# Kernel tuning notes

Hardware: AMD Instinct MI355X
Metric: run time of the kernel (lower is better)

Reference implementation:

```python
import jax, jax.numpy as jnp
import numpy as np

K = 9          # kernel_size
PAD = 4        # padding
N_OUT, C_IN = 32, 32


def setup_inputs() -> dict:
    key = jax.random.key(0)
    k1, k2, k3, k4, k5 = jax.random.split(key, 5)
    x = jax.random.normal(k1, (16, C_IN, 192, 192), jnp.float32)
    sx = jax.random.uniform(k2, (N_OUT, C_IN), jnp.float32, 0.2, 4.0)
    sy = jax.random.uniform(k3, (N_OUT, C_IN), jnp.float32, 0.2, 4.0)
    th = jax.random.uniform(k4, (N_OUT, C_IN), jnp.float32, 0.0, 2.0 * np.pi)
    weight = jnp.stack([sx, sy, th], axis=-1)          # [N, C, 3]
    bias = jax.random.normal(k5, (N_OUT,), jnp.float32) * 0.01
    return {"x": x, "weight": weight, "bias": bias}


def _gaussian_kernels(weight, k):
    # weight: [N, C, 3] -> normalized anisotropic Gaussian kernels [N, C, k, k]
    sx, sy = weight[..., 0], weight[..., 1]
    rad = weight[..., 2] / 180.0 * jnp.pi          # matches theta/180*pi in source
    c, s = jnp.cos(rad), jnp.sin(rad)
    sx2, sy2 = sx * sx, sy * sy
    # Sigma = U diag(sx^2, sy^2) U^T, U = [[c,-s],[s,c]] -> Sigma = [[a,b],[b,d]]
    a = c * c * sx2 + s * s * sy2
    b = c * s * (sx2 - sy2)
    d = s * s * sx2 + c * c * sy2
    det = a * d - b * b
    ia, ib, id_ = d / det, -b / det, a / det       # closed-form 2x2 inverse
    ax = jnp.arange(k, dtype=jnp.float32) - k // 2
    xx = ax[None, :]                               # x varies along columns
    yy = ax[:, None]                               # y varies along rows
    # quadratic form: ia*x^2 + 2*ib*x*y + id*y^2, broadcast to [N, C, k, k]
    q = (ia[..., None, None] * (xx * xx)
         + 2.0 * ib[..., None, None] * (xx * yy)
         + id_[..., None, None] * (yy * yy))
    ker = jnp.exp(-0.5 * q)
    return ker / jnp.sum(ker, axis=(-2, -1), keepdims=True)


def reference(x, weight, bias):
    w = _gaussian_kernels(weight, K)               # [N, C, K, K]
    out = jax.lax.conv_general_dilated(
        x, w, window_strides=(1, 1), padding=[(PAD, PAD), (PAD, PAD)],
        dimension_numbers=("NCHW", "OIHW", "NCHW"))
    return out + bias[None, :, None, None]
```

## Files before the change

### kernel.cpp

```cpp
#include <hip/hip_runtime.h>

#define H 192
#define W 192
#define CIN 32
#define NOUT 32
#define NB 16
#define PADI 4

#define HT 16
#define WTL 16
#define RROWS 24
#define RCOLS 24

typedef __attribute__((ext_vector_type(8))) short bf16x8;
typedef __attribute__((ext_vector_type(4))) float f32x4;

__device__ __forceinline__ unsigned short f2bf(float f) {
    union { float f; unsigned int u; } v; v.f = f;
    unsigned int r = v.u + 0x7fffu + ((v.u >> 16) & 1u);
    return (unsigned short)(r >> 16);
}

__global__ void genw_kernel(const float* __restrict__ wp, unsigned short* __restrict__ W2g) {
    int idx = blockIdx.x * blockDim.x + threadIdx.x;
    if (idx >= NOUT * CIN) return;
    int o = idx / CIN;
    float sx = wp[idx * 3 + 0], sy = wp[idx * 3 + 1], th = wp[idx * 3 + 2];
    float rad = th / 180.0f * 3.14159265358979323846f;
    float co = cosf(rad), si = sinf(rad);
    float sx2 = sx * sx, sy2 = sy * sy;
    float a = co * co * sx2 + si * si * sy2;
    float b = co * si * (sx2 - sy2);
    float d = si * si * sx2 + co * co * sy2;
    float det = a * d - b * b;
    float ia = d / det, ib = -b / det, idd = a / det;
    float ker[81];
    float sum = 0.0f;
    for (int ky = 0; ky < 9; ky++) {
        float yy = (float)(ky - 4);
        for (int kx = 0; kx < 9; kx++) {
            float xx = (float)(kx - 4);
            float q = ia * xx * xx + 2.0f * ib * xx * yy + idd * yy * yy;
            float v = expf(-0.5f * q);
            ker[ky * 9 + kx] = v;
            sum += v;
        }
    }
    float inv = 1.0f / sum;
    int i = idx % CIN;
    int mt = o >> 4, m = o & 15, quad = i >> 3, j = i & 7;
    for (int tap = 0; tap < 81; tap++) {
        W2g[((((mt * 81 + tap) * 4 + quad) * 16 + m) << 3) + j] = f2bf(ker[tap] * inv);
    }
}

__global__ __launch_bounds__(256, 4) void conv_kernel(
    const float* __restrict__ x, const unsigned short* __restrict__ W2g,
    const float* __restrict__ bias, float* __restrict__ out)
{
    __shared__ __align__(16) unsigned short ldsx[4 * RROWS * RCOLS * 8];

    const int t = threadIdx.x;
    const int bid = blockIdx.x;
    const int wb = bid % (W / WTL);
    const int hb = (bid / (W / WTL)) % (H / HT);
    const int n  = bid / ((W / WTL) * (H / HT));
    const int row0 = hb * HT - PADI;
    const int col0 = wb * WTL - PADI;
    const float* xn = x + (size_t)n * CIN * H * W;

    #pragma unroll
    for (int it = 0; it < (4 * RROWS * RCOLS) / 256; ++it) {
        int idx = it * 256 + t;
        int w = idx % RCOLS;
        int r = (idx / RCOLS) % RROWS;
        int quad = idx / (RCOLS * RROWS);
        int row = row0 + r, col = col0 + w;
        unsigned int d[4] = {0u, 0u, 0u, 0u};
        if ((unsigned)row < (unsigned)H && (unsigned)col < (unsigned)W) {
            const float* p = xn + ((size_t)(quad * 8) * H + row) * W + col;
            #pragma unroll
            for (int k = 0; k < 4; k++) {
                float v0 = p[(size_t)(2 * k) * H * W];
                float v1 = p[(size_t)(2 * k + 1) * H * W];
                d[k] = (unsigned int)f2bf(v0) | ((unsigned int)f2bf(v1) << 16);
            }
        }
        *(uint4*)&ldsx[(size_t)idx * 8] = make_uint4(d[0], d[1], d[2], d[3]);
    }
    __syncthreads();

    const int wave = t >> 6;
    const int lane = t & 63;
    const int l15 = lane & 15;
    const int quad4 = lane >> 4;
    const int mt = wave & 1;
    const int rbase = (wave >> 1) * 8;

    f32x4 acc[8];
    #pragma unroll
    for (int i = 0; i < 8; i++) acc[i] = (f32x4){0.f, 0.f, 0.f, 0.f};

    const bf16x8* __restrict__ Wp = (const bf16x8*)W2g;

    for (int dx = 0; dx < 9; dx++) {
        bf16x8 Afr[9];
        #pragma unroll
        for (int dy = 0; dy < 9; dy++) {
            int tap = dy * 9 + dx;
            Afr[dy] = Wp[((mt * 81 + tap) * 4 + quad4) * 16 + l15];
        }
        #pragma unroll
        for (int rr = 0; rr < 16; rr++) {
            const int ldsrow = rbase + rr;
            const bf16x8 bfrag =
                *(const bf16x8*)&ldsx[(size_t)(((quad4 * RROWS + ldsrow) * RCOLS) + (l15 + dx)) * 8];
            #pragma unroll
            for (int dy = 0; dy < 9; dy++) {
                const int orr = rr - dy;
                if (orr >= 0 && orr < 8) {
                    acc[orr] = __builtin_amdgcn_mfma_f32_16x16x32_bf16(
                        Afr[dy], bfrag, acc[orr], 0, 0, 0);
                }
            }
        }
    }

    float* outn = out + (size_t)n * NOUT * H * W;
    float bb[4];
    #pragma unroll
    for (int reg = 0; reg < 4; reg++) bb[reg] = bias[mt * 16 + quad4 * 4 + reg];
    #pragma unroll
    for (int orr = 0; orr < 8; orr++) {
        const int row = hb * HT + rbase + orr;
        const int col = wb * WTL + l15;
        #pragma unroll
        for (int reg = 0; reg < 4; reg++) {
            const int och = mt * 16 + quad4 * 4 + reg;
            outn[((size_t)och * H + row) * W + col] = acc[orr][reg] + bb[reg];
        }
    }
}

extern "C" void kernel_launch(void* const* d_in, const int* in_sizes, int n_in,
                              void* d_out, int out_size, void* d_ws, size_t ws_size,
                              hipStream_t stream) {
    const float* x    = (const float*)d_in[0];
    const float* wp   = (const float*)d_in[1];
    const float* bias = (const float*)d_in[2];
    float* out = (float*)d_out;
    unsigned short* W2g = (unsigned short*)d_ws;

    genw_kernel<<<4, 256, 0, stream>>>(wp, W2g);
    const int blocks = NB * (H / HT) * (W / WTL);
    conv_kernel<<<blocks, 256, 0, stream>>>(x, W2g, bias, out);
}
```

Measured before the change: 211.3 us.

## Parallelize weight generation, swizzle blocks, batch global loads, double-buffer weight fragments

```diff
diff --git a/kernel.cpp b/kernel.cpp
--- a/kernel.cpp
+++ b/kernel.cpp
@@ -22,35 +22,40 @@
 }
 
 __global__ void genw_kernel(const float* __restrict__ wp, unsigned short* __restrict__ W2g) {
-    int idx = blockIdx.x * blockDim.x + threadIdx.x;
-    if (idx >= NOUT * CIN) return;
-    int o = idx / CIN;
-    float sx = wp[idx * 3 + 0], sy = wp[idx * 3 + 1], th = wp[idx * 3 + 2];
+    const int b = blockIdx.x;
+    const int o = b >> 5;
+    const int i = b & 31;
+    const int t = threadIdx.x;
+
+    float sx = wp[b * 3 + 0], sy = wp[b * 3 + 1], th = wp[b * 3 + 2];
     float rad = th / 180.0f * 3.14159265358979323846f;
     float co = cosf(rad), si = sinf(rad);
     float sx2 = sx * sx, sy2 = sy * sy;
     float a = co * co * sx2 + si * si * sy2;
-    float b = co * si * (sx2 - sy2);
+    float bb = co * si * (sx2 - sy2);
     float d = si * si * sx2 + co * co * sy2;
-    float det = a * d - b * b;
-    float ia = d / det, ib = -b / det, idd = a / det;
-    float ker[81];
-    float sum = 0.0f;
-    for (int ky = 0; ky < 9; ky++) {
-        float yy = (float)(ky - 4);
-        for (int kx = 0; kx < 9; kx++) {
-            float xx = (float)(kx - 4);
-            float q = ia * xx * xx + 2.0f * ib * xx * yy + idd * yy * yy;
-            float v = expf(-0.5f * q);
-            ker[ky * 9 + kx] = v;
-            sum += v;
-        }
+    float det = a * d - bb * bb;
+    float ia = d / det, ib = -bb / det, idd = a / det;
+
+    const int tap = t;
+    float e = 0.0f;
+    if (tap < 81) {
+        float xx = (float)(tap % 9 - 4);
+        float yy = (float)(tap / 9 - 4);
+        float q = ia * xx * xx + 2.0f * ib * xx * yy + idd * yy * yy;
+        e = expf(-0.5f * q);
     }
-    float inv = 1.0f / sum;
-    int i = idx % CIN;
-    int mt = o >> 4, m = o & 15, quad = i >> 3, j = i & 7;
-    for (int tap = 0; tap < 81; tap++) {
-        W2g[((((mt * 81 + tap) * 4 + quad) * 16 + m) << 3) + j] = f2bf(ker[tap] * inv);
+    float s = e;
+    #pragma unroll
+    for (int off = 32; off > 0; off >>= 1) s += __shfl_down(s, off);
+    __shared__ float ws[2];
+    if ((t & 63) == 0) ws[t >> 6] = s;
+    __syncthreads();
+    float total = ws[0] + ws[1];
+
+    if (tap < 81) {
+        int mt = o >> 4, m = o & 15, quad = i >> 3, j = i & 7;
+        W2g[((((mt * 81 + tap) * 4 + quad) * 16 + m) << 3) + j] = f2bf(e / total);
     }
 }
 
@@ -61,7 +66,7 @@
     __shared__ __align__(16) unsigned short ldsx[4 * RROWS * RCOLS * 8];
 
     const int t = threadIdx.x;
-    const int bid = blockIdx.x;
+    const int bid = (blockIdx.x & 7) * 288 + (blockIdx.x >> 3);
     const int wb = bid % (W / WTL);
     const int hb = (bid / (W / WTL)) % (H / HT);
     const int n  = bid / ((W / WTL) * (H / HT));
@@ -69,26 +74,31 @@
     const int col0 = wb * WTL - PADI;
     const float* xn = x + (size_t)n * CIN * H * W;
 
+    float v[9][8];
     #pragma unroll
-    for (int it = 0; it < (4 * RROWS * RCOLS) / 256; ++it) {
+    for (int it = 0; it < 9; ++it) {
         int idx = it * 256 + t;
         int w = idx % RCOLS;
         int r = (idx / RCOLS) % RROWS;
         int quad = idx / (RCOLS * RROWS);
         int row = row0 + r, col = col0 + w;
-        unsigned int d[4] = {0u, 0u, 0u, 0u};
+        #pragma unroll
+        for (int k = 0; k < 8; k++) v[it][k] = 0.0f;
         if ((unsigned)row < (unsigned)H && (unsigned)col < (unsigned)W) {
             const float* p = xn + ((size_t)(quad * 8) * H + row) * W + col;
             #pragma unroll
-            for (int k = 0; k < 4; k++) {
-                float v0 = p[(size_t)(2 * k) * H * W];
-                float v1 = p[(size_t)(2 * k + 1) * H * W];
-                d[k] = (unsigned int)f2bf(v0) | ((unsigned int)f2bf(v1) << 16);
-            }
+            for (int k = 0; k < 8; k++) v[it][k] = p[(size_t)k * H * W];
         }
+    }
+    #pragma unroll
+    for (int it = 0; it < 9; ++it) {
+        int idx = it * 256 + t;
+        unsigned int d[4];
+        #pragma unroll
+        for (int k = 0; k < 4; k++)
+            d[k] = (unsigned int)f2bf(v[it][2 * k]) | ((unsigned int)f2bf(v[it][2 * k + 1]) << 16);
         *(uint4*)&ldsx[(size_t)idx * 8] = make_uint4(d[0], d[1], d[2], d[3]);
     }
-    __syncthreads();
 
     const int wave = t >> 6;
     const int lane = t & 63;
@@ -97,30 +107,38 @@
     const int mt = wave & 1;
     const int rbase = (wave >> 1) * 8;
 
+    const bf16x8* __restrict__ Wp = (const bf16x8*)W2g;
+
+    bf16x8 A[2][9];
+    #pragma unroll
+    for (int dy = 0; dy < 9; dy++)
+        A[0][dy] = Wp[((mt * 81 + dy * 9 + 0) * 4 + quad4) * 16 + l15];
+
+    __syncthreads();
+
     f32x4 acc[8];
     #pragma unroll
     for (int i = 0; i < 8; i++) acc[i] = (f32x4){0.f, 0.f, 0.f, 0.f};
 
-    const bf16x8* __restrict__ Wp = (const bf16x8*)W2g;
+    const unsigned short* bptr = &ldsx[(size_t)(((quad4 * RROWS + rbase) * RCOLS) + l15) * 8];
 
+    #pragma unroll
     for (int dx = 0; dx < 9; dx++) {
-        bf16x8 Afr[9];
-        #pragma unroll
-        for (int dy = 0; dy < 9; dy++) {
-            int tap = dy * 9 + dx;
-            Afr[dy] = Wp[((mt * 81 + tap) * 4 + quad4) * 16 + l15];
+        const int cur = dx & 1, nxt = cur ^ 1;
+        if (dx < 8) {
+            #pragma unroll
+            for (int dy = 0; dy < 9; dy++)
+                A[nxt][dy] = Wp[((mt * 81 + dy * 9 + (dx + 1)) * 4 + quad4) * 16 + l15];
         }
         #pragma unroll
         for (int rr = 0; rr < 16; rr++) {
-            const int ldsrow = rbase + rr;
-            const bf16x8 bfrag =
-                *(const bf16x8*)&ldsx[(size_t)(((quad4 * RROWS + ldsrow) * RCOLS) + (l15 + dx)) * 8];
+            const bf16x8 bfrag = *(const bf16x8*)&bptr[(size_t)(rr * RCOLS + dx) * 8];
             #pragma unroll
             for (int dy = 0; dy < 9; dy++) {
                 const int orr = rr - dy;
                 if (orr >= 0 && orr < 8) {
                     acc[orr] = __builtin_amdgcn_mfma_f32_16x16x32_bf16(
-                        Afr[dy], bfrag, acc[orr], 0, 0, 0);
+                        A[cur][dy], bfrag, acc[orr], 0, 0, 0);
                 }
             }
         }
@@ -151,7 +169,7 @@
     float* out = (float*)d_out;
     unsigned short* W2g = (unsigned short*)d_ws;
 
-    genw_kernel<<<4, 256, 0, stream>>>(wp, W2g);
+    genw_kernel<<<NOUT * CIN, 128, 0, stream>>>(wp, W2g);
     const int blocks = NB * (H / HT) * (W / WTL);
     conv_kernel<<<blocks, 256, 0, stream>>>(x, W2g, bias, out);
 }
```

Result: faster. 190.2 us (-10.0%).
